# Optimization experiments

Measured on AMD Instinct MI355X. Metric: run time of the kernel, lower is better.

The kernel has to match this reference:

```python
import jax, jax.numpy as jnp
import numpy as np

EMBED_DIM = 1024
NUM_HEADS = 16
EFF_HEADS = NUM_HEADS // 2
HEAD_DIM = EMBED_DIM // NUM_HEADS
LAMBDA_INIT = 0.8
B, N = 2, 2048


def setup_inputs() -> dict:
    key = jax.random.key(0)
    ks = jax.random.split(key, 14)
    s = 0.02
    return {
        "x": jax.random.normal(ks[0], (B, N, EMBED_DIM), dtype=jnp.float32),
        "Wq": jax.random.normal(ks[1], (EMBED_DIM, EMBED_DIM), dtype=jnp.float32) * s,
        "bq": jnp.zeros((EMBED_DIM,), dtype=jnp.float32),
        "Wk": jax.random.normal(ks[2], (EMBED_DIM, EMBED_DIM), dtype=jnp.float32) * s,
        "bk": jnp.zeros((EMBED_DIM,), dtype=jnp.float32),
        "Wv": jax.random.normal(ks[3], (EMBED_DIM, EMBED_DIM), dtype=jnp.float32) * s,
        "bv": jnp.zeros((EMBED_DIM,), dtype=jnp.float32),
        "Wp": jax.random.normal(ks[4], (EMBED_DIM, EMBED_DIM), dtype=jnp.float32) * s,
        "bp": jnp.zeros((EMBED_DIM,), dtype=jnp.float32),
        "lambda_q1": jax.random.normal(ks[5], (EFF_HEADS, 1, HEAD_DIM), dtype=jnp.float32) * s,
        "lambda_k1": jax.random.normal(ks[6], (EFF_HEADS, 1, HEAD_DIM), dtype=jnp.float32) * s,
        "lambda_q2": jax.random.normal(ks[7], (EFF_HEADS, 1, HEAD_DIM), dtype=jnp.float32) * s,
        "lambda_k2": jax.random.normal(ks[8], (EFF_HEADS, 1, HEAD_DIM), dtype=jnp.float32) * s,
    }


def reference(x, Wq, bq, Wk, bk, Wv, bv, Wp, bp,
              lambda_q1, lambda_k1, lambda_q2, lambda_k2):
    Bb, Nn, C = x.shape
    H, H2, hd = NUM_HEADS, EFF_HEADS, HEAD_DIM
    scale = hd ** (-0.5)

    # projections (torch Linear: y = x @ W.T + b), reshape to [B,H,N,hd]
    q = (x @ Wq.T + bq).reshape(Bb, Nn, H, hd).transpose(0, 2, 1, 3)
    k = (x @ Wk.T + bk).reshape(Bb, Nn, H, hd).transpose(0, 2, 1, 3)
    v = (x @ Wv.T + bv).reshape(Bb, Nn, H, hd).transpose(0, 2, 1, 3)

    q1, q2 = q[:, :H2], q[:, H2:]
    k1, k2 = k[:, :H2], k[:, H2:]
    v1, v2 = v[:, :H2], v[:, H2:]

    # scalar lambda: per-head dot products, clamped exp, differenced, averaged
    l1 = jnp.exp(jnp.minimum((lambda_q1 * lambda_k1).sum((-1, -2)), 5.0))  # [H2]
    l2 = jnp.exp(jnp.minimum((lambda_q2 * lambda_k2).sum((-1, -2)), 5.0))
    lv = (l1 - l2 + LAMBDA_INIT).mean()

    a1 = jax.nn.softmax(jnp.einsum('bhnd,bhmd->bhnm', q1, k1) * scale, axis=-1)
    x1 = jnp.einsum('bhnm,bhmd->bhnd', a1, v1).transpose(0, 2, 1, 3).reshape(Bb, Nn, C // 2)
    a2 = jax.nn.softmax(jnp.einsum('bhnd,bhmd->bhnm', q2, k2) * scale, axis=-1)
    x2 = jnp.einsum('bhnm,bhmd->bhnd', a2, v2).transpose(0, 2, 1, 3).reshape(Bb, Nn, C // 2)

    out = jnp.concatenate([x1 - lv * x2, x2], axis=-1) @ Wp.T + bp
    return out
```

## Files before the change

### kernel.cpp

```cpp
#include <hip/hip_runtime.h>

typedef __bf16 bf16;
typedef __bf16 bf16x8 __attribute__((ext_vector_type(8)));
typedef __bf16 bf16x4 __attribute__((ext_vector_type(4)));
typedef float  f32x16 __attribute__((ext_vector_type(16)));
typedef unsigned int uint;
typedef unsigned int uintx4 __attribute__((ext_vector_type(4)));

#define QSCALE (0.125f * 1.44269504088896340736f)

__device__ __forceinline__ void g2l16(const void* g, void* l) {
  __builtin_amdgcn_global_load_lds(
      (const __attribute__((address_space(1))) void*)g,
      (__attribute__((address_space(3))) void*)l, 16, 0, 0);
}

__device__ __forceinline__ f32x16 mfma16(bf16x8 a, bf16x8 b, f32x16 c) {
  return __builtin_amdgcn_mfma_f32_32x32x16_bf16(a, b, c, 0, 0, 0);
}

__device__ __forceinline__ uint pack_bf16(float a, float b) {
  unsigned short lo = __builtin_bit_cast(unsigned short, (bf16)a);
  unsigned short hi = __builtin_bit_cast(unsigned short, (bf16)b);
  return (uint)lo | ((uint)hi << 16);
}

__global__ void cast5_kernel(const float* __restrict__ x,
                             const float* __restrict__ wq, const float* __restrict__ wk,
                             const float* __restrict__ wv, const float* __restrict__ wp,
                             bf16* __restrict__ xb, bf16* __restrict__ wqkv,
                             bf16* __restrict__ wpb) {
  int seg = blockIdx.y;
  long i = (long)(blockIdx.x * 256 + threadIdx.x) * 8;
  const float* s; bf16* d; long n;
  if (seg == 0)      { s = x;  d = xb;  n = 4194304; }
  else if (seg == 1) { s = wq; d = wqkv;            n = 1048576; }
  else if (seg == 2) { s = wk; d = wqkv + 1048576;  n = 1048576; }
  else if (seg == 3) { s = wv; d = wqkv + 2097152;  n = 1048576; }
  else               { s = wp; d = wpb;             n = 1048576; }
  if (i >= n) return;
  float4 f0 = *(const float4*)(s + i);
  float4 f1 = *(const float4*)(s + i + 4);
  bf16x8 o;
  o[0] = (bf16)f0.x; o[1] = (bf16)f0.y; o[2] = (bf16)f0.z; o[3] = (bf16)f0.w;
  o[4] = (bf16)f1.x; o[5] = (bf16)f1.y; o[6] = (bf16)f1.z; o[7] = (bf16)f1.w;
  *(bf16x8*)(d + i) = o;
}

__global__ void lv_kernel(const float* __restrict__ lq1, const float* __restrict__ lk1,
                          const float* __restrict__ lq2, const float* __restrict__ lk2,
                          float* __restrict__ lvp) {
  int t = threadIdx.x;
  float accum = 0.f;
  for (int hh = 0; hh < 8; ++hh) {
    float v1 = lq1[hh*64 + t] * lk1[hh*64 + t];
    float v2 = lq2[hh*64 + t] * lk2[hh*64 + t];
    for (int off = 32; off; off >>= 1) {
      v1 += __shfl_xor(v1, off);
      v2 += __shfl_xor(v2, off);
    }
    accum += expf(fminf(v1, 5.f)) - expf(fminf(v2, 5.f));
  }
  if (t == 0) *lvp = accum / 8.f + 0.8f;
}

__global__ __launch_bounds__(256, 2) void gemm_qkv_kernel(
    const bf16* __restrict__ A, const bf16* __restrict__ B,
    const float* __restrict__ bias0, const float* __restrict__ bias1,
    const float* __restrict__ bias2,
    bf16* __restrict__ O0, bf16* __restrict__ O1, bf16* __restrict__ O2) {
  __shared__ __align__(16) char smem[32 * 1024];
  const int tid = threadIdx.x;
  const int w = tid >> 6, L = tid & 63;
  const int l31 = L & 31, h5 = L >> 5;
  const int m0 = blockIdx.x * 128;
  const int n0g = blockIdx.y * 128;
  const int by = n0g >> 10;
  const bf16* Bp = B + (long)by * 1048576;
  const float* biasp = (by == 0) ? bias0 : ((by == 1) ? bias1 : bias2);
  const int nloc = n0g & 1023;

  f32x16 acc[2][2];
  for (int i = 0; i < 2; ++i) for (int j = 0; j < 2; ++j)
    for (int r = 0; r < 16; ++r) acc[i][j][r] = 0.f;

  const int srow = L >> 1, spar = L & 1;
  const int wm = w >> 1, wn = w & 1;
  const int fs = (l31 * 2 + h5) * 16;

  for (int k0 = 0; k0 < 1024; k0 += 64) {
    for (int i = 0; i < 8; ++i) {
      int r = w * 8 + i;
      int rr = r & 15;
      int rowblk = rr >> 2, kst = rr & 3;
      int row = rowblk * 32 + srow;
      int kk = k0 + (kst * 2 + spar) * 8;
      const bf16* gsrc = (r < 16) ? (A + (long)(m0 + row) * 1024 + kk)
                                  : (Bp + (long)(nloc + row) * 1024 + kk);
      g2l16(gsrc, smem + r * 1024);
    }
    __syncthreads();
    for (int kst = 0; kst < 4; ++kst) {
      bf16x8 a0 = *(const bf16x8*)(smem + (((wm * 2 + 0) * 4 + kst) * 1024) + fs);
      bf16x8 a1 = *(const bf16x8*)(smem + (((wm * 2 + 1) * 4 + kst) * 1024) + fs);
      bf16x8 b0 = *(const bf16x8*)(smem + 16384 + (((wn * 2 + 0) * 4 + kst) * 1024) + fs);
      bf16x8 b1 = *(const bf16x8*)(smem + 16384 + (((wn * 2 + 1) * 4 + kst) * 1024) + fs);
      acc[0][0] = mfma16(a0, b0, acc[0][0]);
      acc[0][1] = mfma16(a0, b1, acc[0][1]);
      acc[1][0] = mfma16(a1, b0, acc[1][0]);
      acc[1][1] = mfma16(a1, b1, acc[1][1]);
    }
    __syncthreads();
  }

  if (by == 2) {
    int b = m0 >> 11;
    int nbase = (m0 & 2047);
    for (int mi = 0; mi < 2; ++mi) for (int ni = 0; ni < 2; ++ni) {
      int col = nloc + wn * 64 + ni * 32 + l31;
      int hh = col >> 6, d = col & 63;
      float bias_v = biasp[col];
      long rowbase = ((long)(b * 16 + hh) * 64 + d) * 2048
                   + nbase + wm * 64 + mi * 32 + 4 * h5;
      for (int g = 0; g < 4; ++g) {
        bf16x4 pk;
        for (int r = 0; r < 4; ++r) pk[r] = (bf16)(acc[mi][ni][g * 4 + r] + bias_v);
        *(bf16x4*)(O2 + rowbase + 8 * g) = pk;
      }
    }
  } else {
    bf16* dst = (by == 0) ? O0 : O1;
    float scale = (by == 0) ? QSCALE : 1.0f;
    for (int mi = 0; mi < 2; ++mi) for (int ni = 0; ni < 2; ++ni) {
      int col = nloc + wn * 64 + ni * 32 + l31;
      float bias_v = biasp[col];
      int row_base = m0 + wm * 64 + mi * 32 + 4 * h5;
      for (int reg = 0; reg < 16; ++reg) {
        int rowoff = (reg & 3) + 8 * (reg >> 2);
        float v = (acc[mi][ni][reg] + bias_v) * scale;
        dst[(long)(row_base + rowoff) * 1024 + col] = (bf16)v;
      }
    }
  }
}

__global__ __launch_bounds__(256, 2) void gemm_proj_kernel(
    const bf16* __restrict__ A, const bf16* __restrict__ B,
    const float* __restrict__ bias, float* __restrict__ Of) {
  __shared__ __align__(16) char smem[24 * 1024];
  const int tid = threadIdx.x;
  const int w = tid >> 6, L = tid & 63;
  const int l31 = L & 31, h5 = L >> 5;
  const int m0 = blockIdx.x * 64;
  const int nloc = blockIdx.y * 128;

  f32x16 acc[2];
  for (int i = 0; i < 2; ++i)
    for (int r = 0; r < 16; ++r) acc[i][r] = 0.f;

  const int srow = L >> 1, spar = L & 1;
  const int fs = (l31 * 2 + h5) * 16;

  for (int k0 = 0; k0 < 1024; k0 += 64) {
    for (int i = 0; i < 6; ++i) {
      int r = w * 6 + i;
      const bf16* gsrc;
      if (r < 8) {
        int rowblk = r >> 2, kst = r & 3;
        gsrc = A + (long)(m0 + rowblk * 32 + srow) * 1024 + k0 + (kst * 2 + spar) * 8;
      } else {
        int rr = r - 8;
        int rowblk = rr >> 2, kst = rr & 3;
        gsrc = B + (long)(nloc + rowblk * 32 + srow) * 1024 + k0 + (kst * 2 + spar) * 8;
      }
      g2l16(gsrc, smem + r * 1024);
    }
    __syncthreads();
    for (int kst = 0; kst < 4; ++kst) {
      bf16x8 a0 = *(const bf16x8*)(smem + ((0 * 4 + kst) * 1024) + fs);
      bf16x8 a1 = *(const bf16x8*)(smem + ((1 * 4 + kst) * 1024) + fs);
      bf16x8 bb = *(const bf16x8*)(smem + 8192 + ((w * 4 + kst) * 1024) + fs);
      acc[0] = mfma16(a0, bb, acc[0]);
      acc[1] = mfma16(a1, bb, acc[1]);
    }
    __syncthreads();
  }

  for (int mi = 0; mi < 2; ++mi) {
    int col = nloc + w * 32 + l31;
    float bias_v = bias[col];
    int row_base = m0 + mi * 32 + 4 * h5;
    for (int reg = 0; reg < 16; ++reg) {
      int rowoff = (reg & 3) + 8 * (reg >> 2);
      Of[(long)(row_base + rowoff) * 1024 + col] = acc[mi][reg] + bias_v;
    }
  }
}

__global__ __launch_bounds__(256, 2) void attn_kernel(
    const bf16* __restrict__ Qb, const bf16* __restrict__ Kb,
    const bf16* __restrict__ Vt, bf16* __restrict__ Ob) {
  __shared__ __align__(16) char smem[4 * 4352];
  const int tid = threadIdx.x, w = tid >> 6, L = tid & 63;
  const int bh = blockIdx.x, qt = blockIdx.y;
  const int b = bh >> 4, h = bh & 15;
  const int q0 = qt * 128 + w * 32;
  const int l31 = L & 31, h5 = L >> 5;
  const int srow = L >> 1, spar = L & 1;
  const int fs = (l31 * 2 + h5) * 16;

  bf16x8 qf[4];
  for (int kst = 0; kst < 4; ++kst) {
    int q = q0 + l31;
    qf[kst] = *(const bf16x8*)(Qb + (long)(b * 2048 + q) * 1024 + h * 64
                               + kst * 16 + h5 * 8);
  }

  f32x16 o[2];
  for (int i = 0; i < 2; ++i)
    for (int r = 0; r < 16; ++r) o[i][r] = 0.f;
  float lsum = 0.f;

  const bf16* Kbh = Kb + (long)b * 2048 * 1024 + h * 64;
  const bf16* Vth = Vt + (long)bh * 64 * 2048;

  for (int t = 0; t < 32; ++t) {
    int n0 = t * 64;
    for (int i = 0; i < 4; ++i) {
      int r = w * 4 + i;
      if (r < 8) {
        int nkb = r >> 2, kst = r & 3;
        const bf16* g = Kbh + (long)(n0 + nkb * 32 + srow) * 1024 + (kst * 2 + spar) * 8;
        g2l16(g, smem + r * 1024);
      } else {
        int rr = r - 8, db = rr >> 2, kst = rr & 3;
        const bf16* g = Vth + (long)(db * 32 + srow) * 2048 + n0 + (kst * 2 + spar) * 8;
        g2l16(g, smem + 8192 + rr * 1024);
      }
    }
    __syncthreads();

    f32x16 s[2];
    for (int i = 0; i < 2; ++i)
      for (int r = 0; r < 16; ++r) s[i][r] = 0.f;
    for (int kst = 0; kst < 4; ++kst) {
      bf16x8 k0f = *(const bf16x8*)(smem + ((0 * 4 + kst) * 1024) + fs);
      bf16x8 k1f = *(const bf16x8*)(smem + ((4 + kst) * 1024) + fs);
      s[0] = mfma16(k0f, qf[kst], s[0]);
      s[1] = mfma16(k1f, qf[kst], s[1]);
    }

    for (int nki = 0; nki < 2; ++nki)
      for (int r = 0; r < 16; ++r) {
        float p = __builtin_amdgcn_exp2f(s[nki][r]);
        s[nki][r] = p;
        lsum += p;
      }

    for (int kst = 0; kst < 4; ++kst) {
      bf16x8 v0 = *(const bf16x8*)(smem + 8192 + ((0 * 4 + kst) * 1024) + fs);
      bf16x8 v1 = *(const bf16x8*)(smem + 8192 + ((4 + kst) * 1024) + fs);
      int nki = kst >> 1;
      int rbase = (kst & 1) * 8;
      uint p0a = pack_bf16(s[nki][rbase + 0], s[nki][rbase + 1]);
      uint p0b = pack_bf16(s[nki][rbase + 2], s[nki][rbase + 3]);
      uint p1a = pack_bf16(s[nki][rbase + 4], s[nki][rbase + 5]);
      uint p1b = pack_bf16(s[nki][rbase + 6], s[nki][rbase + 7]);
      uint t0 = h5 ? p0a : p1a;
      uint t1 = h5 ? p0b : p1b;
      uint r0 = (uint)__shfl_xor((int)t0, 32);
      uint r1 = (uint)__shfl_xor((int)t1, 32);
      uintx4 uv;
      uv.x = h5 ? r0 : p0a;
      uv.y = h5 ? r1 : p0b;
      uv.z = h5 ? p1a : r0;
      uv.w = h5 ? p1b : r1;
      bf16x8 pf = __builtin_bit_cast(bf16x8, uv);
      o[0] = mfma16(v0, pf, o[0]);
      o[1] = mfma16(v1, pf, o[1]);
    }
    __syncthreads();
  }

  float l = lsum + __shfl_xor(lsum, 32);
  float linv = 1.f / l;

  char* ot = smem + w * 4352;
  for (int di = 0; di < 2; ++di)
    for (int g = 0; g < 4; ++g) {
      bf16x4 pk;
      for (int r = 0; r < 4; ++r)
        pk[r] = (bf16)(o[di][g * 4 + r] * linv);
      int d0 = di * 32 + g * 8 + h5 * 4;
      *(bf16x4*)(ot + (l31 * 68 + d0) * 2) = pk;
    }
  for (int i = 0; i < 4; ++i) {
    int qloc = (L >> 3) + i * 8;
    int cc = L & 7;
    bf16x8 vv = *(const bf16x8*)(ot + (qloc * 68 + cc * 8) * 2);
    int q = q0 - w * 32 + w * 32;
    (void)q;
    *(bf16x8*)(Ob + (long)(b * 2048 + q0 + qloc) * 1024 + h * 64 + cc * 8) = vv;
  }
}

__global__ void combine_kernel(bf16* __restrict__ Ob, const float* __restrict__ lvp) {
  float lv = *lvp;
  int idx = blockIdx.x * 256 + threadIdx.x;
  int row = idx >> 6;
  int j = (idx & 63) * 8;
  bf16x8 o1 = *(const bf16x8*)(Ob + (long)row * 1024 + j);
  bf16x8 o2 = *(const bf16x8*)(Ob + (long)row * 1024 + 512 + j);
  bf16x8 c1;
  for (int e = 0; e < 8; ++e) c1[e] = (bf16)((float)o1[e] - lv * (float)o2[e]);
  *(bf16x8*)(Ob + (long)row * 1024 + j) = c1;
}

extern "C" void kernel_launch(void* const* d_in, const int* in_sizes, int n_in,
                              void* d_out, int out_size, void* d_ws, size_t ws_size,
                              hipStream_t stream) {
  const float* x   = (const float*)d_in[0];
  const float* Wq  = (const float*)d_in[1];
  const float* bq  = (const float*)d_in[2];
  const float* Wk  = (const float*)d_in[3];
  const float* bk  = (const float*)d_in[4];
  const float* Wv  = (const float*)d_in[5];
  const float* bv  = (const float*)d_in[6];
  const float* Wp  = (const float*)d_in[7];
  const float* bp  = (const float*)d_in[8];
  const float* lq1 = (const float*)d_in[9];
  const float* lk1 = (const float*)d_in[10];
  const float* lq2 = (const float*)d_in[11];
  const float* lk2 = (const float*)d_in[12];
  float* out = (float*)d_out;

  char* ws = (char*)d_ws;
  float* lvp = (float*)ws;
  bf16* xb   = (bf16*)(ws + 1024);
  bf16* Wqkv = xb + (long)4096 * 1024;
  bf16* Wpb  = Wqkv + (long)3 * 1024 * 1024;
  bf16* Vt   = Wpb + (long)1024 * 1024;
  bf16* Ob   = Vt + (long)4096 * 1024;
  bf16* Qb = (bf16*)d_out;
  bf16* Kb = Qb + (long)4096 * 1024;

  cast5_kernel<<<dim3(2048, 5), 256, 0, stream>>>(x, Wq, Wk, Wv, Wp, xb, Wqkv, Wpb);
  lv_kernel<<<1, 64, 0, stream>>>(lq1, lk1, lq2, lk2, lvp);
  gemm_qkv_kernel<<<dim3(32, 24), 256, 0, stream>>>(
      xb, Wqkv, bq, bk, bv, Qb, Kb, Vt);
  attn_kernel<<<dim3(32, 16), 256, 0, stream>>>(Qb, Kb, Vt, Ob);
  combine_kernel<<<1024, 256, 0, stream>>>(Ob, lvp);
  gemm_proj_kernel<<<dim3(64, 8), 256, 0, stream>>>(Ob, Wpb, bp, out);
}
```

Measured before the change: 210.1 us.

## Split key range across two wave groups per attention block and merge via LDS

The attention block grows from 256 to 512 threads. Each half of the waves handles half of the 2048 keys for the same 128 queries, with its own LDS staging area for K and V tiles. At the end the upper half writes its partial O accumulators and row sums to LDS, and the lower half adds them, normalises and stores. This doubles the resident waves per CU to hide load and MFMA latency better, at the cost of an extra LDS reduction and higher register and LDS pressure per block.

```diff
diff --git a/kernel.cpp b/kernel.cpp
--- a/kernel.cpp
+++ b/kernel.cpp
@@ -197,45 +197,45 @@
   }
 }
 
-__global__ __launch_bounds__(256, 2) void attn_kernel(
+__global__ __launch_bounds__(512, 4) void attn_kernel(
     const bf16* __restrict__ Qb, const bf16* __restrict__ Kb,
     const bf16* __restrict__ Vt, bf16* __restrict__ Ob) {
-  __shared__ __align__(16) char smem[4 * 4352];
+  __shared__ __align__(16) char smem[34816];
   const int tid = threadIdx.x, w = tid >> 6, L = tid & 63;
+  const int half = w >> 2, pair = w & 3;
   const int bh = blockIdx.x, qt = blockIdx.y;
   const int b = bh >> 4, h = bh & 15;
-  const int q0 = qt * 128 + w * 32;
+  const int q0 = qt * 128 + pair * 32;
   const int l31 = L & 31, h5 = L >> 5;
   const int srow = L >> 1, spar = L & 1;
   const int fs = (l31 * 2 + h5) * 16;
+  char* kbase = smem + half * 16384;
 
   bf16x8 qf[4];
-  for (int kst = 0; kst < 4; ++kst) {
-    int q = q0 + l31;
-    qf[kst] = *(const bf16x8*)(Qb + (long)(b * 2048 + q) * 1024 + h * 64
+  for (int kst = 0; kst < 4; ++kst)
+    qf[kst] = *(const bf16x8*)(Qb + (long)(b * 2048 + q0 + l31) * 1024 + h * 64
                                + kst * 16 + h5 * 8);
-  }
 
   f32x16 o[2];
   for (int i = 0; i < 2; ++i)
     for (int r = 0; r < 16; ++r) o[i][r] = 0.f;
   float lsum = 0.f;
 
-  const bf16* Kbh = Kb + (long)b * 2048 * 1024 + h * 64;
-  const bf16* Vth = Vt + (long)bh * 64 * 2048;
-
-  for (int t = 0; t < 32; ++t) {
+  const bf16* Kbh = Kb + (long)b * 2048 * 1024 + h * 64 + (long)half * 1024 * 1024;
+  const bf16* Vth = Vt + (long)bh * 64 * 2048 + half * 1024;
+
+  for (int t = 0; t < 16; ++t) {
     int n0 = t * 64;
     for (int i = 0; i < 4; ++i) {
-      int r = w * 4 + i;
+      int r = pair * 4 + i;
       if (r < 8) {
         int nkb = r >> 2, kst = r & 3;
         const bf16* g = Kbh + (long)(n0 + nkb * 32 + srow) * 1024 + (kst * 2 + spar) * 8;
-        g2l16(g, smem + r * 1024);
+        g2l16(g, kbase + r * 1024);
       } else {
         int rr = r - 8, db = rr >> 2, kst = rr & 3;
         const bf16* g = Vth + (long)(db * 32 + srow) * 2048 + n0 + (kst * 2 + spar) * 8;
-        g2l16(g, smem + 8192 + rr * 1024);
+        g2l16(g, kbase + 8192 + rr * 1024);
       }
     }
     __syncthreads();
@@ -244,8 +244,8 @@
     for (int i = 0; i < 2; ++i)
       for (int r = 0; r < 16; ++r) s[i][r] = 0.f;
     for (int kst = 0; kst < 4; ++kst) {
-      bf16x8 k0f = *(const bf16x8*)(smem + ((0 * 4 + kst) * 1024) + fs);
-      bf16x8 k1f = *(const bf16x8*)(smem + ((4 + kst) * 1024) + fs);
+      bf16x8 k0f = *(const bf16x8*)(kbase + ((0 * 4 + kst) * 1024) + fs);
+      bf16x8 k1f = *(const bf16x8*)(kbase + ((4 + kst) * 1024) + fs);
       s[0] = mfma16(k0f, qf[kst], s[0]);
       s[1] = mfma16(k1f, qf[kst], s[1]);
     }
@@ -258,8 +258,8 @@
       }
 
     for (int kst = 0; kst < 4; ++kst) {
-      bf16x8 v0 = *(const bf16x8*)(smem + 8192 + ((0 * 4 + kst) * 1024) + fs);
-      bf16x8 v1 = *(const bf16x8*)(smem + 8192 + ((4 + kst) * 1024) + fs);
+      bf16x8 v0 = *(const bf16x8*)(kbase + 8192 + ((0 * 4 + kst) * 1024) + fs);
+      bf16x8 v1 = *(const bf16x8*)(kbase + 8192 + ((4 + kst) * 1024) + fs);
       int nki = kst >> 1;
       int rbase = (kst & 1) * 8;
       uint p0a = pack_bf16(s[nki][rbase + 0], s[nki][rbase + 1]);
@@ -282,25 +282,39 @@
     __syncthreads();
   }
 
-  float l = lsum + __shfl_xor(lsum, 32);
-  float linv = 1.f / l;
-
-  char* ot = smem + w * 4352;
-  for (int di = 0; di < 2; ++di)
-    for (int g = 0; g < 4; ++g) {
-      bf16x4 pk;
-      for (int r = 0; r < 4; ++r)
-        pk[r] = (bf16)(o[di][g * 4 + r] * linv);
-      int d0 = di * 32 + g * 8 + h5 * 4;
-      *(bf16x4*)(ot + (l31 * 68 + d0) * 2) = pk;
-    }
-  for (int i = 0; i < 4; ++i) {
-    int qloc = (L >> 3) + i * 8;
-    int cc = L & 7;
-    bf16x8 vv = *(const bf16x8*)(ot + (qloc * 68 + cc * 8) * 2);
-    int q = q0 - w * 32 + w * 32;
-    (void)q;
-    *(bf16x8*)(Ob + (long)(b * 2048 + q0 + qloc) * 1024 + h * 64 + cc * 8) = vv;
+  float lcol = lsum + __shfl_xor(lsum, 32);
+  if (half) {
+    float* dstO = (float*)smem + pair * 2112;
+    for (int di = 0; di < 2; ++di)
+      for (int r = 0; r < 16; ++r) dstO[L * 33 + di * 16 + r] = o[di][r];
+    if (h5 == 0) ((float*)(smem + 33792))[pair * 32 + l31] = lcol;
+  }
+  __syncthreads();
+  float linv = 0.f;
+  if (!half) {
+    float* srcO = (float*)smem + pair * 2112;
+    for (int di = 0; di < 2; ++di)
+      for (int r = 0; r < 16; ++r) o[di][r] += srcO[L * 33 + di * 16 + r];
+    float lother = ((float*)(smem + 33792))[pair * 32 + l31];
+    linv = 1.f / (lcol + lother);
+  }
+  __syncthreads();
+  if (!half) {
+    char* ot = smem + pair * 4352;
+    for (int di = 0; di < 2; ++di)
+      for (int g = 0; g < 4; ++g) {
+        bf16x4 pk;
+        for (int r = 0; r < 4; ++r)
+          pk[r] = (bf16)(o[di][g * 4 + r] * linv);
+        int d0 = di * 32 + g * 8 + h5 * 4;
+        *(bf16x4*)(ot + (l31 * 68 + d0) * 2) = pk;
+      }
+    for (int i = 0; i < 4; ++i) {
+      int qloc = (L >> 3) + i * 8;
+      int cc = L & 7;
+      bf16x8 vv = *(const bf16x8*)(ot + (qloc * 68 + cc * 8) * 2);
+      *(bf16x8*)(Ob + (long)(b * 2048 + q0 + qloc) * 1024 + h * 64 + cc * 8) = vv;
+    }
   }
 }
 
@@ -348,7 +362,7 @@
   lv_kernel<<<1, 64, 0, stream>>>(lq1, lk1, lq2, lk2, lvp);
   gemm_qkv_kernel<<<dim3(32, 24), 256, 0, stream>>>(
       xb, Wqkv, bq, bk, bv, Qb, Kb, Vt);
-  attn_kernel<<<dim3(32, 16), 256, 0, stream>>>(Qb, Kb, Vt, Ob);
+  attn_kernel<<<dim3(32, 16), 512, 0, stream>>>(Qb, Kb, Vt, Ob);
   combine_kernel<<<1024, 256, 0, stream>>>(Ob, lvp);
   gemm_proj_kernel<<<dim3(64, 8), 256, 0, stream>>>(Ob, Wpb, bp, out);
 }
```

Measured after the change: 210.0 us. About the same (-0.0%).
